# Kernel tuning notes

Hardware: AMD Instinct MI355X
Metric: run time of the kernel (lower is better)

The kernel has to match this reference:

```python
import jax, jax.numpy as jnp
import numpy as np

EMB = 512
HEADS = 8


def setup_inputs() -> dict:
    key = jax.random.key(0)
    ks = jax.random.split(key, 9)
    b, t, k, h = 4, 2048, EMB, HEADS
    s = 1.0 / np.sqrt(k)
    x = jax.random.normal(ks[0], (b, t, k), dtype=jnp.float32)
    Wq = jax.random.normal(ks[1], (k, h * k), dtype=jnp.float32) * s
    bq = jnp.zeros((h * k,), dtype=jnp.float32)
    Wk = jax.random.normal(ks[2], (k, h * k), dtype=jnp.float32) * s
    bk = jnp.zeros((h * k,), dtype=jnp.float32)
    Wv = jax.random.normal(ks[3], (k, h * k), dtype=jnp.float32) * s
    bv = jnp.zeros((h * k,), dtype=jnp.float32)
    Wo = jax.random.normal(ks[4], (h * k, k), dtype=jnp.float32) * (1.0 / np.sqrt(h * k))
    bo = jnp.zeros((k,), dtype=jnp.float32)
    return {"x": x, "Wq": Wq, "bq": bq, "Wk": Wk, "bk": bk,
            "Wv": Wv, "bv": bv, "Wo": Wo, "bo": bo}


def reference(x, Wq, bq, Wk, bk, Wv, bv, Wo, bo):
    b, t, k = x.shape
    h = Wq.shape[1] // k
    scale = k ** (-0.25)  # applied to both q and k, matching /= k**(1/4)
    # projections: [b,t,k] -> [b,t,h,k] -> [b,h,t,k]
    q = (x @ Wq + bq).reshape(b, t, h, k).transpose(0, 2, 1, 3) * scale
    kk = (x @ Wk + bk).reshape(b, t, h, k).transpose(0, 2, 1, 3) * scale
    v = (x @ Wv + bv).reshape(b, t, h, k).transpose(0, 2, 1, 3)
    # attention scores [b,h,t,t]
    scores = jnp.einsum('bhqk,bhsk->bhqs', q, kk)
    w = jax.nn.softmax(scores, axis=-1)
    out = jnp.einsum('bhqs,bhsk->bhqk', w, v)  # [b,h,t,k]
    out = out.transpose(0, 2, 1, 3).reshape(b, t, h * k)
    return out @ Wo + bo
```

## Files before the change

### kernel.cpp

```cpp
#include <hip/hip_runtime.h>
#include <hip/hip_bf16.h>
#include <stdint.h>

typedef __hip_bfloat16 bf16;
typedef __bf16 bf16x8 __attribute__((ext_vector_type(8)));
typedef float floatx4 __attribute__((ext_vector_type(4)));

#define AS_LDS __attribute__((address_space(3)))
#define AS_GLB __attribute__((address_space(1)))

__device__ __forceinline__ void gload_lds16(const bf16* g, bf16* l) {
    __builtin_amdgcn_global_load_lds((const AS_GLB void*)g, (AS_LDS void*)l, 16, 0, 0);
}

__global__ void probe_dtype(const float* __restrict__ x, int* __restrict__ flag) {
    __shared__ int cnt;
    if (threadIdx.x == 0) cnt = 0;
    __syncthreads();
    int ok = 0;
    for (int i = threadIdx.x; i < 4096; i += 256) {
        float v = x[i];
        if (v == v && fabsf(v) < 1.0e3f) ok++;
    }
    atomicAdd(&cnt, ok);
    __syncthreads();
    if (threadIdx.x == 0) *flag = (cnt > 2048) ? 1 : 0;
}

__global__ __launch_bounds__(256) void zero_f32(float* __restrict__ p, int n) {
    int i = blockIdx.x * 256 + threadIdx.x;
    if (i < n) p[i] = 0.f;
}

__global__ __launch_bounds__(256) void convert_to_bf16(
    const void* __restrict__ in, bf16* __restrict__ out, long n,
    const int* __restrict__ flag)
{
    long i = ((long)blockIdx.x * 256 + threadIdx.x) * 8;
    if (i >= n) return;
    bf16 o[8];
    if (*flag) {
        const float* p = (const float*)in + i;
        float4 a = *(const float4*)p;
        float4 b = *(const float4*)(p + 4);
        o[0] = __float2bfloat16(a.x); o[1] = __float2bfloat16(a.y);
        o[2] = __float2bfloat16(a.z); o[3] = __float2bfloat16(a.w);
        o[4] = __float2bfloat16(b.x); o[5] = __float2bfloat16(b.y);
        o[6] = __float2bfloat16(b.z); o[7] = __float2bfloat16(b.w);
    } else {
        *(float4*)o = *(const float4*)((const bf16*)in + i);
    }
    *(float4*)&out[i] = *(float4*)o;
}

__global__ __launch_bounds__(256) void emit_out(
    const bf16* __restrict__ in, void* __restrict__ out, long n,
    const int* __restrict__ flag)
{
    long i = ((long)blockIdx.x * 256 + threadIdx.x) * 8;
    if (i >= n) return;
    bf16 v[8];
    *(float4*)v = *(const float4*)&in[i];
    if (*flag) {
        float* o = (float*)out + i;
        float4 a, b;
        a.x = __bfloat162float(v[0]); a.y = __bfloat162float(v[1]);
        a.z = __bfloat162float(v[2]); a.w = __bfloat162float(v[3]);
        b.x = __bfloat162float(v[4]); b.y = __bfloat162float(v[5]);
        b.z = __bfloat162float(v[6]); b.w = __bfloat162float(v[7]);
        *(float4*)o = a;
        *(float4*)(o + 4) = b;
    } else {
        *(float4*)((bf16*)out + i) = *(float4*)v;
    }
}

__global__ __launch_bounds__(256) void transpose_any(
    const void* __restrict__ inv, bf16* __restrict__ out,
    int ldin, int ldout, const int* __restrict__ flag)
{
    __shared__ bf16 tile[64][80];
    const int fp32 = *flag;
    const int c0 = blockIdx.x * 64;
    const int r0 = blockIdx.y * 64;
    const int tid = threadIdx.x;
#pragma unroll
    for (int it = 0; it < 2; ++it) {
        int ch = tid + it * 256;
        int r = ch >> 3, c = (ch & 7) * 8;
        long eidx = (long)(r0 + r) * ldin + (c0 + c);
        if (fp32) {
            const float* p = (const float*)inv + eidx;
            float4 a = *(const float4*)p;
            float4 b = *(const float4*)(p + 4);
            bf16 o[8];
            o[0] = __float2bfloat16(a.x); o[1] = __float2bfloat16(a.y);
            o[2] = __float2bfloat16(a.z); o[3] = __float2bfloat16(a.w);
            o[4] = __float2bfloat16(b.x); o[5] = __float2bfloat16(b.y);
            o[6] = __float2bfloat16(b.z); o[7] = __float2bfloat16(b.w);
            *(float4*)&tile[r][c] = *(float4*)o;
        } else {
            *(float4*)&tile[r][c] = *(const float4*)((const bf16*)inv + eidx);
        }
    }
    __syncthreads();
#pragma unroll
    for (int it = 0; it < 2; ++it) {
        int ch = tid + it * 256;
        int oc = ch >> 3, rb = (ch & 7) * 8;
        bf16 tmp[8];
#pragma unroll
        for (int i = 0; i < 8; ++i) tmp[i] = tile[rb + i][oc];
        *(float4*)&out[(long)(c0 + oc) * ldout + r0 + rb] = *(float4*)tmp;
    }
}

__global__ __launch_bounds__(256) void transpose_bf16(
    const bf16* __restrict__ in, bf16* __restrict__ out,
    int ldin, int ldout,
    int nz1, long in_z1, long out_z1, long in_z2, long out_z2)
{
    __shared__ bf16 tile[64][80];
    const int z = blockIdx.z;
    const int z1 = z % nz1, z2 = z / nz1;
    in  += (long)z1 * in_z1 + (long)z2 * in_z2;
    out += (long)z1 * out_z1 + (long)z2 * out_z2;
    const int c0 = blockIdx.x * 64;
    const int r0 = blockIdx.y * 64;
    const int tid = threadIdx.x;
#pragma unroll
    for (int it = 0; it < 2; ++it) {
        int ch = tid + it * 256;
        int r = ch >> 3, c = (ch & 7) * 8;
        *(float4*)&tile[r][c] = *(const float4*)&in[(long)(r0 + r) * ldin + c0 + c];
    }
    __syncthreads();
#pragma unroll
    for (int it = 0; it < 2; ++it) {
        int ch = tid + it * 256;
        int oc = ch >> 3, rb = (ch & 7) * 8;
        bf16 tmp[8];
#pragma unroll
        for (int i = 0; i < 8; ++i) tmp[i] = tile[rb + i][oc];
        *(float4*)&out[(long)(c0 + oc) * ldout + r0 + rb] = *(float4*)tmp;
    }
}

template <int MODE, int SWZ>
__global__ __launch_bounds__(512, 2) void gemm256(
    const bf16* __restrict__ A, const bf16* __restrict__ Bt,
    bf16* __restrict__ C, const bf16* __restrict__ bias,
    int lda, int ldb, int ldc,
    long az, long bz, long cz, int K, float scale, int qcols,
    bf16* __restrict__ Vt, int vcol0, float* __restrict__ Lsum)
{
    __shared__ bf16 AsL[2][2][256 * 32];
    __shared__ bf16 BsL[2][2][256 * 32];

    const int tid  = threadIdx.x;
    const int lane = tid & 63;
    const int wave = tid >> 6;
    const int wr = wave >> 2;
    const int wc = wave & 3;
    const int lm = lane & 15;
    const int cl = lane >> 4;

    int bxx = blockIdx.x, byy = blockIdx.y, bzz = blockIdx.z;
    if constexpr (SWZ == 1) {
        int flat = bxx + (byy << 3) + (bzz << 6);
        int xcd = flat & 7, idx = flat >> 3;
        bzz = xcd; bxx = idx & 7; byy = idx >> 3;
    } else if constexpr (SWZ == 2) {
        int flat = bxx + byy * 48;
        int xcd = flat & 7, idx = flat >> 3;
        bxx = xcd * 6 + idx % 6; byy = idx / 6; bzz = 0;
    }
    const long zz = bzz;
    A  += zz * az;
    Bt += zz * bz;
    C  += zz * cz;
    float* Lz = (MODE == 1) ? (Lsum + zz * 2048) : nullptr;
    const int m0 = byy * 256;
    const int n0 = bxx * 256;

    int offA[8], offB[4];
#pragma unroll
    for (int i = 0; i < 8; ++i) {
        int row = wr * 128 + i * 16 + lm;
        offA[i] = row * 32 + ((cl ^ ((row >> 1) & 3)) << 3);
    }
#pragma unroll
    for (int j = 0; j < 4; ++j) {
        int row = wc * 64 + j * 16 + lm;
        offB[j] = row * 32 + ((cl ^ ((row >> 1) & 3)) << 3);
    }

    const int sr = lane >> 2;
    const int sc = lane & 3;
    const int NT = K >> 6;

    floatx4 acc[8][4];
#pragma unroll
    for (int i = 0; i < 8; ++i)
#pragma unroll
        for (int j = 0; j < 4; ++j)
            acc[i][j] = (floatx4){0.f, 0.f, 0.f, 0.f};

    auto stageU = [&](int which, int t, int kh) {
        if (t >= NT) return;
        const bf16* G = which ? Bt : A;
        const int ldg  = which ? ldb : lda;
        const int g0   = which ? n0 : m0;
        bf16* lb = which ? &BsL[t & 1][kh][0] : &AsL[t & 1][kh][0];
        const int kcol = t * 64 + kh * 32;
#pragma unroll
        for (int ii = 0; ii < 2; ++ii) {
            int row = ii * 128 + wave * 16 + sr;
            int cg  = sc ^ ((row >> 1) & 3);
            gload_lds16(G + (long)(g0 + row) * ldg + kcol + cg * 8,
                        lb + row * 32 + sc * 8);
        }
    };

    bf16x8 af[8], bfv[2];
    auto dsA = [&](int b, int kh) {
        const bf16* p = &AsL[b][kh][0];
#pragma unroll
        for (int i = 0; i < 8; ++i) af[i] = *(const bf16x8*)(p + offA[i]);
    };
    auto dsB = [&](int b, int kh, int nh) {
        const bf16* p = &BsL[b][kh][0];
        bfv[0] = *(const bf16x8*)(p + offB[nh * 2]);
        bfv[1] = *(const bf16x8*)(p + offB[nh * 2 + 1]);
    };
    auto mfmaQ = [&](int nh) {
        __builtin_amdgcn_s_setprio(1);
#pragma unroll
        for (int i = 0; i < 8; ++i) {
            acc[i][nh * 2] = __builtin_amdgcn_mfma_f32_16x16x32_bf16(
                af[i], bfv[0], acc[i][nh * 2], 0, 0, 0);
            acc[i][nh * 2 + 1] = __builtin_amdgcn_mfma_f32_16x16x32_bf16(
                af[i], bfv[1], acc[i][nh * 2 + 1], 0, 0, 0);
        }
        __builtin_amdgcn_s_setprio(0);
    };

#define BAR    __builtin_amdgcn_s_barrier()
#define SBZ    __builtin_amdgcn_sched_barrier(0)
#define LGKM0  do { asm volatile("s_waitcnt lgkmcnt(0)" ::: "memory"); SBZ; } while (0)
#define VM(n)  do { asm volatile("s_waitcnt vmcnt(" #n ")" ::: "memory"); SBZ; } while (0)

    stageU(0, 0, 0); stageU(1, 0, 0); stageU(0, 0, 1); stageU(1, 0, 1);
    stageU(0, 1, 0); stageU(1, 1, 0);
    VM(4);
    BAR;

    for (int t0 = 0; t0 < NT; t0 += 2) {
        const bool last = (t0 + 2 >= NT);
        dsA(0, 0); dsB(0, 0, 0); stageU(0, t0 + 1, 1);
        BAR; LGKM0; mfmaQ(0); BAR;
        dsB(0, 0, 1); stageU(1, t0 + 1, 1);
        BAR; LGKM0; mfmaQ(1); BAR;
        dsA(0, 1); dsB(0, 1, 0); stageU(0, t0 + 2, 0);
        BAR; LGKM0; mfmaQ(0); BAR;
        dsB(0, 1, 1); stageU(1, t0 + 2, 0);
        BAR; LGKM0; mfmaQ(1);
        if (last) { VM(0); } else { VM(4); }
        BAR;
        dsA(1, 0); dsB(1, 0, 0); stageU(0, t0 + 2, 1);
        BAR; LGKM0; mfmaQ(0); BAR;
        dsB(1, 0, 1); stageU(1, t0 + 2, 1);
        BAR; LGKM0; mfmaQ(1); BAR;
        dsA(1, 1); dsB(1, 1, 0); stageU(0, t0 + 3, 0);
        BAR; LGKM0; mfmaQ(0); BAR;
        dsB(1, 1, 1); stageU(1, t0 + 3, 0);
        BAR; LGKM0; mfmaQ(1);
        if (!last) { VM(4); }
        BAR;
    }
#undef BAR
#undef SBZ
#undef LGKM0
#undef VM

    const int cr = (lane >> 4) * 4;
    if constexpr (MODE == 1) {
#pragma unroll
        for (int j = 0; j < 4; ++j) {
            long q = n0 + wc * 64 + j * 16 + lm;
            bf16* Cr = C + q * ldc + m0 + wr * 128;
            float rs = 0.f;
#pragma unroll
            for (int i = 0; i < 8; ++i) {
                bf16 pk[4];
#pragma unroll
                for (int r = 0; r < 4; ++r) {
                    float e = __expf(acc[i][j][r]);
                    rs += e;
                    pk[r] = __float2bfloat16(e);
                }
                *(uint64_t*)&Cr[i * 16 + cr] = *(const uint64_t*)pk;
            }
            rs += __shfl_xor(rs, 16);
            rs += __shfl_xor(rs, 32);
            if (cl == 0) atomicAdd(&Lz[q], rs);
        }
    } else {
        if (n0 >= vcol0) {
#pragma unroll
            for (int j = 0; j < 4; ++j) {
                int col = n0 + wc * 64 + j * 16 + lm;
                float bv = __bfloat162float(bias[col]);
                int eg = col - vcol0;
                bf16* vt = Vt + ((long)(eg >> 9) * 512 + (eg & 511)) * 2048;
#pragma unroll
                for (int i = 0; i < 8; ++i) {
                    int t0v = m0 + wr * 128 + i * 16 + cr;
                    bf16 pk[4];
#pragma unroll
                    for (int r = 0; r < 4; ++r)
                        pk[r] = __float2bfloat16(acc[i][j][r] + bv);
                    *(uint64_t*)&vt[t0v] = *(const uint64_t*)pk;
                }
            }
        } else {
            const int l4 = lane & 3;
            float bvj[4], scj[4];
#pragma unroll
            for (int j = 0; j < 4; ++j) {
                int col = n0 + wc * 64 + j * 16 + lm;
                bvj[j] = __bfloat162float(bias[col]);
                scj[j] = (col < qcols) ? scale : 1.0f;
            }
#pragma unroll
            for (int i = 0; i < 8; ++i) {
                int row = m0 + wr * 128 + i * 16 + cr + l4;
                bf16* Cr = C + (long)row * ldc + n0 + wc * 64 + (lm & ~3);
#pragma unroll
                for (int j = 0; j < 4; ++j) {
                    float x0 = (acc[i][j][0] + bvj[j]) * scj[j];
                    float x1 = (acc[i][j][1] + bvj[j]) * scj[j];
                    float x2 = (acc[i][j][2] + bvj[j]) * scj[j];
                    float x3 = (acc[i][j][3] + bvj[j]) * scj[j];
                    float u = __shfl_xor((l4 & 1) ? x0 : x1, 1);
                    float v = __shfl_xor((l4 & 1) ? x2 : x3, 1);
                    if (l4 & 1) { x0 = u; x2 = v; } else { x1 = u; x3 = v; }
                    u = __shfl_xor((l4 & 2) ? x0 : x2, 2);
                    v = __shfl_xor((l4 & 2) ? x1 : x3, 2);
                    if (l4 & 2) { x0 = u; x1 = v; } else { x2 = u; x3 = v; }
                    bf16 pk[4];
                    pk[0] = __float2bfloat16(x0); pk[1] = __float2bfloat16(x1);
                    pk[2] = __float2bfloat16(x2); pk[3] = __float2bfloat16(x3);
                    *(uint64_t*)&Cr[j * 16] = *(const uint64_t*)pk;
                }
            }
        }
    }
}

__global__ __launch_bounds__(512, 2) void gemm_pv(
    const bf16* __restrict__ A, const bf16* __restrict__ Bt,
    bf16* __restrict__ C, const float* __restrict__ L,
    int lda, int ldb, int ldc, long az, long bz, long cz, int K)
{
    __shared__ bf16 AsL[2][2][512 * 32];
    __shared__ bf16 BsL[2][64 * 64];

    const int tid  = threadIdx.x;
    const int lane = tid & 63;
    const int wave = tid >> 6;
    const int wm = wave >> 1;
    const int wn = wave & 1;
    const int lm = lane & 15;
    const int cl = lane >> 4;

    int flat = blockIdx.x + (blockIdx.z << 5);
    const long zz = flat & 7;
    const int qt = flat >> 3;
    A  += zz * az;
    Bt += zz * bz;
    C  += zz * cz;
    const float* Lz = L + zz * 2048;
    const int n0 = qt * 64;

    int offA[8];
#pragma unroll
    for (int i = 0; i < 8; ++i) {
        int row = wm * 128 + i * 16 + lm;
        offA[i] = row * 32 + ((cl ^ ((row >> 1) & 3)) << 3);
    }
    int rB[2], gB0[2];
#pragma unroll
    for (int j = 0; j < 2; ++j) {
        rB[j] = wn * 32 + j * 16 + lm;
        gB0[j] = rB[j] & 7;
    }

    const int sr = lane >> 2;
    const int sc = lane & 3;
    const int NT = K >> 6;

    floatx4 acc[8][2];
#pragma unroll
    for (int i = 0; i < 8; ++i)
#pragma unroll
        for (int j = 0; j < 2; ++j)
            acc[i][j] = (floatx4){0.f, 0.f, 0.f, 0.f};

    auto stageA = [&](int t, int kh) {
        if (t >= NT) return;
        bf16* lb = &AsL[t & 1][kh][0];
        const int kcol = t * 64 + kh * 32;
#pragma unroll
        for (int seg = 0; seg < 4; ++seg) {
            int row = seg * 128 + wave * 16 + sr;
            int cg  = sc ^ ((row >> 1) & 3);
            gload_lds16(A + (long)row * lda + kcol + cg * 8,
                        lb + row * 32 + sc * 8);
        }
    };
    auto stageB = [&](int t) {
        if (t >= NT) return;
        bf16* lb = &BsL[t & 1][0];
        const int kcol = t * 64;
        int row = wave * 8 + (lane >> 3);
        int cg  = (lane & 7) ^ (row & 7);
        gload_lds16(Bt + (long)(n0 + row) * ldb + kcol + cg * 8,
                    lb + row * 64 + (lane & 7) * 8);
    };

    bf16x8 af[8], bfv[2];
    auto dsA = [&](int b, int kh) {
        const bf16* p = &AsL[b][kh][0];
#pragma unroll
        for (int i = 0; i < 8; ++i) af[i] = *(const bf16x8*)(p + offA[i]);
    };
    auto dsB = [&](int b, int kh) {
        const bf16* p = &BsL[b][0];
#pragma unroll
        for (int j = 0; j < 2; ++j) {
            int g = (kh * 4 + cl) ^ gB0[j];
            bfv[j] = *(const bf16x8*)(p + rB[j] * 64 + g * 8);
        }
    };
    auto mfmaQ = [&]() {
        __builtin_amdgcn_s_setprio(1);
#pragma unroll
        for (int i = 0; i < 8; ++i) {
            acc[i][0] = __builtin_amdgcn_mfma_f32_16x16x32_bf16(
                af[i], bfv[0], acc[i][0], 0, 0, 0);
            acc[i][1] = __builtin_amdgcn_mfma_f32_16x16x32_bf16(
                af[i], bfv[1], acc[i][1], 0, 0, 0);
        }
        __builtin_amdgcn_s_setprio(0);
    };

#define BAR    __builtin_amdgcn_s_barrier()
#define SBZ    __builtin_amdgcn_sched_barrier(0)
#define LGKM0  do { asm volatile("s_waitcnt lgkmcnt(0)" ::: "memory"); SBZ; } while (0)
#define VM(n)  do { asm volatile("s_waitcnt vmcnt(" #n ")" ::: "memory"); SBZ; } while (0)

    stageA(0, 0); stageB(0); stageA(0, 1); stageA(1, 0);
    VM(4);
    BAR;

    for (int t0 = 0; t0 < NT; t0 += 2) {
        const bool last = (t0 + 2 >= NT);
        dsA(0, 0); dsB(0, 0); stageA(t0 + 1, 1); stageB(t0 + 1);
        BAR; LGKM0; mfmaQ(); BAR;
        dsA(0, 1); dsB(0, 1); stageA(t0 + 2, 0);
        BAR; LGKM0; mfmaQ();
        if (last) { VM(0); } else { VM(4); }
        BAR;
        dsA(1, 0); dsB(1, 0); stageA(t0 + 2, 1); stageB(t0 + 2);
        BAR; LGKM0; mfmaQ(); BAR;
        dsA(1, 1); dsB(1, 1); stageA(t0 + 3, 0);
        BAR; LGKM0; mfmaQ();
        if (!last) { VM(4); }
        BAR;
    }
#undef BAR
#undef SBZ
#undef LGKM0
#undef VM

#pragma unroll
    for (int j = 0; j < 2; ++j) {
        int col = n0 + wn * 32 + j * 16 + lm;
        float inv = 1.0f / Lz[col];
        bf16* Cr = C + (long)col * ldc + wm * 128;
#pragma unroll
        for (int i = 0; i < 8; ++i) {
            bf16 pk[4];
#pragma unroll
            for (int r = 0; r < 4; ++r)
                pk[r] = __float2bfloat16(acc[i][j][r] * inv);
            *(uint64_t*)&Cr[i * 16 + cl * 4] = *(const uint64_t*)pk;
        }
    }
}

template <int MODE, int SWZ>
__global__ __launch_bounds__(512, 2) void gemm128n(
    const bf16* __restrict__ A, const bf16* __restrict__ Bt,
    bf16* __restrict__ C, const float* __restrict__ L,
    int lda, int ldb, int ldc,
    long az, long bz, long cz, int K, int kper)
{
    __shared__ bf16 AsL[2][2][128 * 32];
    __shared__ bf16 BsL[2][2][256 * 32];

    const int tid  = threadIdx.x;
    const int lane = tid & 63;
    const int wave = tid >> 6;
    const int wr = wave >> 2;
    const int wc = wave & 3;
    const int lm = lane & 15;
    const int cl = lane >> 4;

    int bxx = blockIdx.x, byy = blockIdx.y, bzz = blockIdx.z;
    if constexpr (SWZ == 5) {
        int flat = bxx + (byy << 3) + (bzz << 5);
        int xcd = flat & 7, idx = flat >> 3;
        bzz = xcd; bxx = idx & 7; byy = idx >> 3;
    } else if constexpr (SWZ == 6) {
        int flat = bxx + (byy << 5) + (bzz << 7);
        int nf = (flat & 7) * 32 + (flat >> 3);
        bzz = nf >> 7; int rr = nf & 127; byy = rr >> 5; bxx = rr & 31;
    }
    const long zz = bzz;
    A  += zz * az;
    Bt += zz * bz;
    C  += zz * cz;
    const float* Lz = (MODE == 5) ? (L + zz * 2048) : nullptr;
    const int kbase = (int)(zz * (long)kper);
    const int m0 = byy * 128;
    const int n0 = bxx * 256;

    int offA[4], offB[4];
#pragma unroll
    for (int i = 0; i < 4; ++i) {
        int row = wr * 64 + i * 16 + lm;
        offA[i] = row * 32 + ((cl ^ ((row >> 1) & 3)) << 3);
    }
#pragma unroll
    for (int j = 0; j < 4; ++j) {
        int row = wc * 64 + j * 16 + lm;
        offB[j] = row * 32 + ((cl ^ ((row >> 1) & 3)) << 3);
    }

    const int sr = lane >> 2;
    const int sc = lane & 3;
    const int NT = K >> 6;

    floatx4 acc[4][4];
#pragma unroll
    for (int i = 0; i < 4; ++i)
#pragma unroll
        for (int j = 0; j < 4; ++j)
            acc[i][j] = (floatx4){0.f, 0.f, 0.f, 0.f};

    auto stageA = [&](int t, int kh) {
        if (t >= NT) return;
        bf16* lb = &AsL[t & 1][kh][0];
        const int kcol = kbase + t * 64 + kh * 32;
        int row = wave * 16 + sr;
        int cg  = sc ^ ((row >> 1) & 3);
        gload_lds16(A + (long)(m0 + row) * lda + kcol + cg * 8,
                    lb + row * 32 + sc * 8);
    };
    auto stageB = [&](int t, int kh) {
        if (t >= NT) return;
        bf16* lb = &BsL[t & 1][kh][0];
        const int kcol = kbase + t * 64 + kh * 32;
#pragma unroll
        for (int ii = 0; ii < 2; ++ii) {
            int row = ii * 128 + wave * 16 + sr;
            int cg  = sc ^ ((row >> 1) & 3);
            gload_lds16(Bt + (long)(n0 + row) * ldb + kcol + cg * 8,
                        lb + row * 32 + sc * 8);
        }
    };

    bf16x8 af[4], bfv[2];
    auto dsA = [&](int b, int kh) {
        const bf16* p = &AsL[b][kh][0];
#pragma unroll
        for (int i = 0; i < 4; ++i) af[i] = *(const bf16x8*)(p + offA[i]);
    };
    auto dsB = [&](int b, int kh, int nh) {
        const bf16* p = &BsL[b][kh][0];
        bfv[0] = *(const bf16x8*)(p + offB[nh * 2]);
        bfv[1] = *(const bf16x8*)(p + offB[nh * 2 + 1]);
    };
    auto mfmaQ = [&](int nh) {
        __builtin_amdgcn_s_setprio(1);
#pragma unroll
        for (int i = 0; i < 4; ++i) {
            acc[i][nh * 2] = __builtin_amdgcn_mfma_f32_16x16x32_bf16(
                af[i], bfv[0], acc[i][nh * 2], 0, 0, 0);
            acc[i][nh * 2 + 1] = __builtin_amdgcn_mfma_f32_16x16x32_bf16(
                af[i], bfv[1], acc[i][nh * 2 + 1], 0, 0, 0);
        }
        __builtin_amdgcn_s_setprio(0);
    };

#define BAR    __builtin_amdgcn_s_barrier()
#define SBZ    __builtin_amdgcn_sched_barrier(0)
#define LGKM0  do { asm volatile("s_waitcnt lgkmcnt(0)" ::: "memory"); SBZ; } while (0)
#define VM(n)  do { asm volatile("s_waitcnt vmcnt(" #n ")" ::: "memory"); SBZ; } while (0)

    stageA(0, 0); stageB(0, 0); stageA(0, 1); stageB(0, 1);
    stageA(1, 0); stageB(1, 0);
    VM(3);
    BAR;

    for (int t0 = 0; t0 < NT; t0 += 2) {
        const bool last = (t0 + 2 >= NT);
        dsA(0, 0); dsB(0, 0, 0); stageA(t0 + 1, 1);
        BAR; LGKM0; mfmaQ(0); BAR;
        dsB(0, 0, 1); stageB(t0 + 1, 1);
        BAR; LGKM0; mfmaQ(1); BAR;
        dsA(0, 1); dsB(0, 1, 0); stageA(t0 + 2, 0);
        BAR; LGKM0; mfmaQ(0); BAR;
        dsB(0, 1, 1); stageB(t0 + 2, 0);
        BAR; LGKM0; mfmaQ(1);
        if (last) { VM(0); } else { VM(3); }
        BAR;
        dsA(1, 0); dsB(1, 0, 0); stageA(t0 + 2, 1);
        BAR; LGKM0; mfmaQ(0); BAR;
        dsB(1, 0, 1); stageB(t0 + 2, 1);
        BAR; LGKM0; mfmaQ(1); BAR;
        dsA(1, 1); dsB(1, 1, 0); stageA(t0 + 3, 0);
        BAR; LGKM0; mfmaQ(0); BAR;
        dsB(1, 1, 1); stageB(t0 + 3, 0);
        BAR; LGKM0; mfmaQ(1);
        if (!last) { VM(3); }
        BAR;
    }
#undef BAR
#undef SBZ
#undef LGKM0
#undef VM

    const int cr = cl * 4;
#pragma unroll
    for (int j = 0; j < 4; ++j) {
        int col = n0 + wc * 64 + j * 16 + lm;
        bf16* Cr = C + (long)col * ldc + m0 + wr * 64;
        float inv = 1.0f;
        if constexpr (MODE == 5) inv = 1.0f / Lz[col];
#pragma unroll
        for (int i = 0; i < 4; ++i) {
            bf16 pk[4];
#pragma unroll
            for (int r = 0; r < 4; ++r)
                pk[r] = __float2bfloat16(acc[i][j][r] * inv);
            *(uint64_t*)&Cr[i * 16 + cr] = *(const uint64_t*)pk;
        }
    }
}

template <int MODE, bool SWAP = false, int SWZ = 0>
__global__ __launch_bounds__(256) void gemm_bt(
    const bf16* __restrict__ A, const bf16* __restrict__ Bt,
    bf16* __restrict__ C, const bf16* __restrict__ bias,
    int lda, int ldb, int ldc,
    long az, long bz, long cz, int K, float scale, int qcols,
    bf16* __restrict__ Vt, int vcol0)
{
    __shared__ bf16 As[128 * 64];
    __shared__ bf16 Bs[128 * 64];

    const int tid  = threadIdx.x;
    const int lane = tid & 63;
    const int wave = tid >> 6;
    const int wx = wave & 1;
    const int wy = wave >> 1;

    int bxx = blockIdx.x, byy = blockIdx.y, bzz = blockIdx.z;
    const long zz = bzz;
    A  += zz * az;
    Bt += zz * bz;
    C  += zz * cz;
    const int bm = SWAP ? bxx : byy;
    const int bn = SWAP ? byy : bxx;
    const int m0 = bm * 128;
    const int n0 = bn * 128;

    const int lm = lane & 15;
    const int kq = (lane >> 4) * 8;

    floatx4 acc[4][4];
#pragma unroll
    for (int i = 0; i < 4; ++i)
#pragma unroll
        for (int j = 0; j < 4; ++j)
            acc[i][j] = (floatx4){0.f, 0.f, 0.f, 0.f};

    for (int kt = 0; kt < K; kt += 64) {
        __syncthreads();
#pragma unroll
        for (int it = 0; it < 4; ++it) {
            int ch = tid + it * 256;
            int r = ch >> 3;
            int c = (ch & 7) * 8;
            gload_lds16(A  + (long)(m0 + r) * lda + (kt + c), &As[ch * 8]);
            gload_lds16(Bt + (long)(n0 + r) * ldb + (kt + c), &Bs[ch * 8]);
        }
        __syncthreads();
#pragma unroll
        for (int kk = 0; kk < 64; kk += 32) {
            bf16x8 af[4], bfv[4];
#pragma unroll
            for (int i = 0; i < 4; ++i)
                af[i] = *(const bf16x8*)&As[(wy * 64 + i * 16 + lm) * 64 + kk + kq];
#pragma unroll
            for (int j = 0; j < 4; ++j)
                bfv[j] = *(const bf16x8*)&Bs[(wx * 64 + j * 16 + lm) * 64 + kk + kq];
#pragma unroll
            for (int i = 0; i < 4; ++i)
#pragma unroll
                for (int j = 0; j < 4; ++j)
                    acc[i][j] = __builtin_amdgcn_mfma_f32_16x16x32_bf16(
                        af[i], bfv[j], acc[i][j], 0, 0, 0);
        }
    }

    const int cr = (lane >> 4) * 4;
    if constexpr (MODE == 1) {
#pragma unroll
        for (int j = 0; j < 4; ++j) {
            int col = n0 + wx * 64 + j * 16 + lm;
#pragma unroll
            for (int i = 0; i < 4; ++i)
#pragma unroll
                for (int r = 0; r < 4; ++r) {
                    int row = m0 + wy * 64 + i * 16 + cr + r;
                    C[(long)row * ldc + col] = __float2bfloat16(__expf(acc[i][j][r]));
                }
        }
    } else {
#pragma unroll
        for (int j = 0; j < 4; ++j) {
            int col = n0 + wx * 64 + j * 16 + lm;
            float bv = (MODE == 0 && bias) ? __bfloat162float(bias[col]) : 0.f;
            float sc = (col < qcols) ? scale : 1.0f;
#pragma unroll
            for (int i = 0; i < 4; ++i) {
#pragma unroll
                for (int r = 0; r < 4; ++r) {
                    int row = m0 + wy * 64 + i * 16 + cr + r;
                    long idx = (long)row * ldc + col;
                    float v;
                    if (MODE == 2) v = acc[i][j][r] + __bfloat162float(C[idx]);
                    else           v = (acc[i][j][r] + bv) * sc;
                    C[idx] = __float2bfloat16(v);
                }
            }
        }
    }
}

template <bool SWAP = false>
__global__ __launch_bounds__(256) void gemm_bt_splitk(
    const bf16* __restrict__ A, const bf16* __restrict__ Bt,
    bf16* __restrict__ P, int lda, int ldb, int ldp,
    long az, long bz, long pz, long skStride, int nsk, int Kc)
{
    __shared__ bf16 As[128 * 64];
    __shared__ bf16 Bs[128 * 64];

    const int tid  = threadIdx.x;
    const int lane = tid & 63;
    const int wave = tid >> 6;
    const int wx = wave & 1;
    const int wy = wave >> 1;
    const int zz = blockIdx.z;
    const int ks = zz % nsk;
    const int zh = zz / nsk;
    A  += (long)zh * az;
    Bt += (long)zh * bz;
    bf16* Pz = P + (long)zh * pz + (long)ks * skStride;
    const int bm = SWAP ? blockIdx.x : blockIdx.y;
    const int bn = SWAP ? blockIdx.y : blockIdx.x;
    const int m0 = bm * 128;
    const int n0 = bn * 128;
    const int k0 = ks * Kc;

    const int lm = lane & 15;
    const int kq = (lane >> 4) * 8;

    floatx4 acc[4][4];
#pragma unroll
    for (int i = 0; i < 4; ++i)
#pragma unroll
        for (int j = 0; j < 4; ++j)
            acc[i][j] = (floatx4){0.f, 0.f, 0.f, 0.f};

    for (int kt = k0; kt < k0 + Kc; kt += 64) {
        __syncthreads();
#pragma unroll
        for (int it = 0; it < 4; ++it) {
            int ch = tid + it * 256;
            int r = ch >> 3;
            int c = (ch & 7) * 8;
            gload_lds16(A  + (long)(m0 + r) * lda + (kt + c), &As[ch * 8]);
            gload_lds16(Bt + (long)(n0 + r) * ldb + (kt + c), &Bs[ch * 8]);
        }
        __syncthreads();
#pragma unroll
        for (int kk = 0; kk < 64; kk += 32) {
            bf16x8 af[4], bfv[4];
#pragma unroll
            for (int i = 0; i < 4; ++i)
                af[i] = *(const bf16x8*)&As[(wy * 64 + i * 16 + lm) * 64 + kk + kq];
#pragma unroll
            for (int j = 0; j < 4; ++j)
                bfv[j] = *(const bf16x8*)&Bs[(wx * 64 + j * 16 + lm) * 64 + kk + kq];
#pragma unroll
            for (int i = 0; i < 4; ++i)
#pragma unroll
                for (int j = 0; j < 4; ++j)
                    acc[i][j] = __builtin_amdgcn_mfma_f32_16x16x32_bf16(
                        af[i], bfv[j], acc[i][j], 0, 0, 0);
        }
    }

    const int cr = (lane >> 4) * 4;
#pragma unroll
    for (int j = 0; j < 4; ++j) {
        int col = n0 + wx * 64 + j * 16 + lm;
#pragma unroll
        for (int i = 0; i < 4; ++i)
#pragma unroll
            for (int r = 0; r < 4; ++r) {
                int row = m0 + wy * 64 + i * 16 + cr + r;
                Pz[(long)row * ldp + col] = __float2bfloat16(acc[i][j][r]);
            }
    }
}

__global__ __launch_bounds__(256) void reduce_emit(
    const bf16* __restrict__ P, const bf16* __restrict__ bias,
    void* __restrict__ out, long MN, int N,
    const int* __restrict__ flag)
{
    long i = ((long)blockIdx.x * 256 + threadIdx.x) * 8;
    if (i >= MN) return;
    bf16 bb[8], a[8], b[8];
    *(float4*)bb = *(const float4*)&bias[i & (N - 1)];
    *(float4*)a  = *(const float4*)&P[i];
    *(float4*)b  = *(const float4*)&P[MN + i];
    float s[8];
#pragma unroll
    for (int k = 0; k < 8; ++k)
        s[k] = __bfloat162float(bb[k]) + __bfloat162float(a[k]) + __bfloat162float(b[k]);
    if (*flag) {
        float* o = (float*)out + i;
        float4 lo = {s[0], s[1], s[2], s[3]};
        float4 hi = {s[4], s[5], s[6], s[7]};
        *(float4*)o = lo;
        *(float4*)(o + 4) = hi;
    } else {
        bf16 o[8];
#pragma unroll
        for (int k = 0; k < 8; ++k) o[k] = __float2bfloat16(s[k]);
        *(float4*)&((bf16*)out)[i] = *(float4*)o;
    }
}

__global__ __launch_bounds__(256) void reduce_splitk(
    const bf16* __restrict__ P, const bf16* __restrict__ bias,
    bf16* __restrict__ Out, long MN, int N, int SK)
{
    long i = ((long)blockIdx.x * 256 + threadIdx.x) * 8;
    if (i >= MN) return;
    float s[8];
    if (bias) {
        bf16 bb[8];
        *(float4*)bb = *(const float4*)&bias[i & (N - 1)];
#pragma unroll
        for (int k = 0; k < 8; ++k) s[k] = __bfloat162float(bb[k]);
    } else {
#pragma unroll
        for (int k = 0; k < 8; ++k) s[k] = 0.f;
    }
    for (int z = 0; z < SK; ++z) {
        bf16 a[8];
        *(float4*)a = *(const float4*)&P[(long)z * MN + i];
#pragma unroll
        for (int k = 0; k < 8; ++k) s[k] += __bfloat162float(a[k]);
    }
    bf16 o[8];
#pragma unroll
    for (int k = 0; k < 8; ++k) o[k] = __float2bfloat16(s[k]);
    *(float4*)&Out[i] = *(float4*)o;
}

__global__ __launch_bounds__(256) void softmax_rows2048(bf16* __restrict__ S)
{
    __shared__ float red[8];
    const long row = blockIdx.x;
    bf16* p = S + row * 2048;
    const int tid = threadIdx.x;
    float4 raw = *(const float4*)&p[tid * 8];
    bf16 vb[8];
    *(float4*)vb = raw;
    float v[8];
#pragma unroll
    for (int i = 0; i < 8; ++i) v[i] = __bfloat162float(vb[i]);
    float m = v[0];
#pragma unroll
    for (int i = 1; i < 8; ++i) m = fmaxf(m, v[i]);
#pragma unroll
    for (int o = 32; o > 0; o >>= 1) m = fmaxf(m, __shfl_xor(m, o));
    if ((tid & 63) == 0) red[tid >> 6] = m;
    __syncthreads();
    m = fmaxf(fmaxf(red[0], red[1]), fmaxf(red[2], red[3]));
    float s = 0.f;
#pragma unroll
    for (int i = 0; i < 8; ++i) { v[i] = __expf(v[i] - m); s += v[i]; }
#pragma unroll
    for (int o = 32; o > 0; o >>= 1) s += __shfl_xor(s, o);
    if ((tid & 63) == 0) red[4 + (tid >> 6)] = s;
    __syncthreads();
    s = (red[4] + red[5]) + (red[6] + red[7]);
    float inv = 1.f / s;
#pragma unroll
    for (int i = 0; i < 8; ++i) vb[i] = __float2bfloat16(v[i] * inv);
    *(float4*)&p[tid * 8] = *(float4*)vb;
}

extern "C" void kernel_launch(void* const* d_in, const int* in_sizes, int n_in,
                              void* d_out, int out_size, void* d_ws, size_t ws_size,
                              hipStream_t stream)
{
    const int Bb = 4, T = 2048, E = 512, H = 8;
    const int HE = H * E;
    const int N3 = 3 * HE;
    const int N2 = 2 * HE;
    const int M  = Bb * T;
    const long NX = (long)M * E;

    const void* xr = nullptr;
    const void* Wr[4] = {nullptr, nullptr, nullptr, nullptr};
    const void* br[3] = {nullptr, nullptr, nullptr};
    const void* bor = nullptr;
    int nw = 0, nb = 0;
    for (int i = 0; i < n_in; ++i) {
        int s = in_sizes[i];
        if      (s == (int)NX)      xr = d_in[i];
        else if (s == E * HE)       { if (nw < 4) Wr[nw++] = d_in[i]; }
        else if (s == HE)           { if (nb < 3) br[nb++] = d_in[i]; }
        else if (s == E)            bor = d_in[i];
    }
    if (!xr || nw < 4 || nb < 3 || !bor) {
        xr = d_in[0]; Wr[0] = d_in[1]; br[0] = d_in[2]; Wr[1] = d_in[3];
        br[1] = d_in[4]; Wr[2] = d_in[5]; br[2] = d_in[6]; Wr[3] = d_in[7];
        bor = d_in[8];
    }

    const float qscale = 0.04419417382415922f;
    const int   QC = 1 << 30;
    dim3 blk(256);

    bf16* pool = (bf16*)d_ws;
    int*  flag = (int*)(void*)pool;
    bf16* xc   = pool + 8;
    bf16* bqc  = xc  + NX;
    bf16* bkc  = bqc + HE;
    bf16* bvc  = bkc + HE;
    bf16* boc  = bvc + HE;
    bf16* WqT  = boc + E;
    const size_t w2m = (size_t)E * HE;
    bf16* WkT  = WqT + w2m;
    bf16* WvT  = WkT + w2m;
    bf16* WoT  = WvT + w2m;
    bf16* Ofin = WoT + w2m;
    bf16* p0   = Ofin + NX;

    const size_t wsE    = ws_size / sizeof(bf16);
    const size_t fixedE = (size_t)(p0 - pool);
    const size_t wQK   = (size_t)T * N2;
    const size_t wQKV  = (size_t)T * N3;
    const size_t wBat  = (size_t)T * HE;
    const size_t wHd   = (size_t)T * E;
    const size_t sAll  = (size_t)H * T * T;
    const size_t sOne  = (size_t)T * T;
    const size_t wBig  = (size_t)M * HE;
    const size_t wL    = 32768;
    const size_t needB2 = fixedE + wQK + wBat + sAll + wBig + wL;
    const size_t needB  = fixedE + wQKV + 2 * wBat + sAll;
    const size_t needC  = fixedE + 5 * wBat + sOne;
    const size_t needD  = fixedE + 5 * wHd  + sOne;
    if (wsE < needD) return;

    probe_dtype<<<dim3(1), blk, 0, stream>>>((const float*)xr, flag);
    convert_to_bf16<<<dim3((unsigned)((NX / 8 + 255) / 256)), blk, 0, stream>>>(
        xr, xc, NX, flag);
    convert_to_bf16<<<dim3(2), blk, 0, stream>>>(br[0], bqc, HE, flag);
    convert_to_bf16<<<dim3(2), blk, 0, stream>>>(br[1], bkc, HE, flag);
    convert_to_bf16<<<dim3(2), blk, 0, stream>>>(br[2], bvc, HE, flag);
    convert_to_bf16<<<dim3(1), blk, 0, stream>>>(bor, boc, E, flag);
    transpose_any<<<dim3(HE / 64, E / 64, 1), blk, 0, stream>>>(Wr[0], WqT, HE, E, flag);
    transpose_any<<<dim3(HE / 64, E / 64, 1), blk, 0, stream>>>(Wr[1], WkT, HE, E, flag);
    transpose_any<<<dim3(HE / 64, E / 64, 1), blk, 0, stream>>>(Wr[2], WvT, HE, E, flag);
    transpose_any<<<dim3(E / 64, HE / 64, 1), blk, 0, stream>>>(Wr[3], WoT, E, HE, flag);

    if (wsE >= needB2) {
        bf16* QKb = p0;
        bf16* Vtb = QKb + wQK;
        bf16* S   = Vtb + wBat;
        bf16* Oatt = S + sAll;
        float* Lbuf = (float*)(Oatt + wBig);

        for (int b = 0; b < Bb; ++b) {
            const bf16* xb = xc + (size_t)b * T * E;
            gemm256<4, 2><<<dim3(N3 / 256, T / 256, 1), dim3(512), 0, stream>>>(
                xb, WqT, QKb, bqc, E, E, N2, 0, 0, 0, E, qscale, HE, Vtb, N2,
                nullptr);
            zero_f32<<<dim3(64), blk, 0, stream>>>(Lbuf, H * T);
            gemm256<1, 1><<<dim3(T / 256, T / 256, H), dim3(512), 0, stream>>>(
                QKb + HE, QKb, S, nullptr, N2, N2, T,
                (long)E, (long)E, (long)T * T, E, 1.f, QC, nullptr, 0, Lbuf);
            gemm_pv<<<dim3(T / 64, 1, H), dim3(512), 0, stream>>>(
                Vtb, S, Oatt + (size_t)b * T * HE, Lbuf, T, T, HE,
                (long)E * T, (long)T * T, (long)E, T);
        }
        gemm128n<6, 6><<<dim3(M / 256, E / 128, 2), dim3(512), 0, stream>>>(
            WoT, Oatt, QKb, nullptr, HE, HE, E,
            0, 0, (long)M * E, HE / 2, HE / 2);
        reduce_emit<<<dim3((unsigned)((NX / 8 + 255) / 256)), blk, 0, stream>>>(
            QKb, boc, d_out, NX, E, flag);
        return;
    }

    if (wsE >= needB) {
        bf16* QKVb = p0;
        bf16* Vtb  = QKVb + wQKV;
        bf16* Oatt = Vtb + wBat;
        bf16* S    = Oatt + wBat;

        for (int b = 0; b < Bb; ++b) {
            const bf16* xb = xc + (size_t)b * T * E;
            gemm_bt<0><<<dim3(N3 / 128, T / 128, 1), blk, 0, stream>>>(
                xb, WqT, QKVb, bqc, E, E, N3, 0, 0, 0, E, qscale, HE, nullptr, 0);
            transpose_bf16<<<dim3(E / 64, T / 64, H), blk, 0, stream>>>(
                QKVb + 2 * HE, Vtb, N3, T, H, (long)E, (long)E * T, 0, 0);
            gemm_bt<0><<<dim3(T / 128, T / 128, H), blk, 0, stream>>>(
                QKVb, QKVb + HE, S, nullptr, N3, N3, T,
                (long)E, (long)E, (long)T * T, E, 1.f, QC, nullptr, 0);
            softmax_rows2048<<<dim3(H * T, 1, 1), blk, 0, stream>>>(S);
            gemm_bt<0><<<dim3(E / 128, T / 128, H), blk, 0, stream>>>(
                S, Vtb, Oatt, nullptr, T, T, HE,
                (long)T * T, (long)E * T, (long)E, T, 1.f, QC, nullptr, 0);
            gemm_bt_splitk<false><<<dim3(E / 128, T / 128, 8), blk, 0, stream>>>(
                Oatt, WoT, (bf16*)S, HE, HE, E, 0, 0, 0, (long)T * E, 8, HE / 8);
            reduce_splitk<<<dim3((unsigned)(((long)T * E / 8 + 255) / 256)), blk, 0, stream>>>(
                (bf16*)S, boc, Ofin + (size_t)b * T * E, (long)T * E, E, 8);
        }
    } else if (wsE >= needC) {
        bf16* Qb  = p0;
        bf16* Kb  = Qb  + wBat;
        bf16* Vb  = Kb  + wBat;
        bf16* Vtb = Vb  + wBat;
        bf16* Ob  = Vtb + wBat;
        bf16* S   = Ob  + wBat;

        for (int b = 0; b < Bb; ++b) {
            const bf16* xb = xc + (size_t)b * T * E;
            gemm_bt<0><<<dim3(HE / 128, T / 128, 1), blk, 0, stream>>>(
                xb, WqT, Qb, bqc, E, E, HE, 0, 0, 0, E, qscale, QC, nullptr, 0);
            gemm_bt<0><<<dim3(HE / 128, T / 128, 1), blk, 0, stream>>>(
                xb, WkT, Kb, bkc, E, E, HE, 0, 0, 0, E, 1.f, QC, nullptr, 0);
            gemm_bt<0><<<dim3(HE / 128, T / 128, 1), blk, 0, stream>>>(
                xb, WvT, Vb, bvc, E, E, HE, 0, 0, 0, E, 1.f, QC, nullptr, 0);
            transpose_bf16<<<dim3(E / 64, T / 64, H), blk, 0, stream>>>(
                Vb, Vtb, HE, T, H, (long)E, (long)E * T, 0, 0);
            for (int h = 0; h < H; ++h) {
                gemm_bt<0><<<dim3(T / 128, T / 128, 1), blk, 0, stream>>>(
                    Qb + (size_t)h * E, Kb + (size_t)h * E, S, nullptr,
                    HE, HE, T, 0, 0, 0, E, 1.f, QC, nullptr, 0);
                softmax_rows2048<<<dim3(T, 1, 1), blk, 0, stream>>>(S);
                gemm_bt<0><<<dim3(E / 128, T / 128, 1), blk, 0, stream>>>(
                    S, Vtb + (size_t)h * E * T, Ob + (size_t)h * E, nullptr,
                    T, T, HE, 0, 0, 0, T, 1.f, QC, nullptr, 0);
            }
            gemm_bt<0><<<dim3(E / 128, T / 128, 1), blk, 0, stream>>>(
                Ob, WoT, Ofin + (size_t)b * T * E, boc,
                HE, HE, E, 0, 0, 0, HE, 1.f, QC, nullptr, 0);
        }
    } else {
        bf16* Qh  = p0;
        bf16* Kh  = Qh  + wHd;
        bf16* Vh  = Kh  + wHd;
        bf16* Vth = Vh  + wHd;
        bf16* Oh  = Vth + wHd;
        bf16* S   = Oh  + wHd;

        for (int b = 0; b < Bb; ++b) {
            const bf16* xb = xc + (size_t)b * T * E;
            bf16* outb = Ofin + (size_t)b * T * E;
            for (int h = 0; h < H; ++h) {
                const size_t hw = (size_t)h * E * E;
                gemm_bt<0><<<dim3(E / 128, T / 128, 1), blk, 0, stream>>>(
                    xb, WqT + hw, Qh, bqc + (size_t)h * E, E, E, E,
                    0, 0, 0, E, qscale, QC, nullptr, 0);
                gemm_bt<0><<<dim3(E / 128, T / 128, 1), blk, 0, stream>>>(
                    xb, WkT + hw, Kh, bkc + (size_t)h * E, E, E, E,
                    0, 0, 0, E, 1.f, QC, nullptr, 0);
                gemm_bt<0><<<dim3(E / 128, T / 128, 1), blk, 0, stream>>>(
                    xb, WvT + hw, Vh, bvc + (size_t)h * E, E, E, E,
                    0, 0, 0, E, 1.f, QC, nullptr, 0);
                transpose_bf16<<<dim3(E / 64, T / 64, 1), blk, 0, stream>>>(
                    Vh, Vth, E, T, 1, 0, 0, 0, 0);
                gemm_bt<0><<<dim3(T / 128, T / 128, 1), blk, 0, stream>>>(
                    Qh, Kh, S, nullptr, E, E, T, 0, 0, 0, E, 1.f, QC, nullptr, 0);
                softmax_rows2048<<<dim3(T, 1, 1), blk, 0, stream>>>(S);
                gemm_bt<0><<<dim3(E / 128, T / 128, 1), blk, 0, stream>>>(
                    S, Vth, Oh, nullptr, T, T, E, 0, 0, 0, T, 1.f, QC, nullptr, 0);
                if (h == 0)
                    gemm_bt<0><<<dim3(E / 128, T / 128, 1), blk, 0, stream>>>(
                        Oh, WoT, outb, boc, E, HE, E, 0, 0, 0, E, 1.f, QC, nullptr, 0);
                else
                    gemm_bt<2><<<dim3(E / 128, T / 128, 1), blk, 0, stream>>>(
                        Oh, WoT + (size_t)h * E, outb, nullptr,
                        E, HE, E, 0, 0, 0, E, 1.f, QC, nullptr, 0);
            }
        }
    }

    emit_out<<<dim3((unsigned)((NX / 8 + 255) / 256)), blk, 0, stream>>>(
        Ofin, d_out, NX, flag);
}
```

Baseline: 981.0 us.

## Retile PV GEMM to 256x256 output blocks with split A/B staging

```diff
diff --git a/kernel.cpp b/kernel.cpp
--- a/kernel.cpp
+++ b/kernel.cpp
@@ -358,75 +358,69 @@
     }
 }
 
-__global__ __launch_bounds__(512, 2) void gemm_pv(
+__global__ __launch_bounds__(512, 2) void gemm_pv3(
     const bf16* __restrict__ A, const bf16* __restrict__ Bt,
     bf16* __restrict__ C, const float* __restrict__ L,
     int lda, int ldb, int ldc, long az, long bz, long cz, int K)
 {
-    __shared__ bf16 AsL[2][2][512 * 32];
-    __shared__ bf16 BsL[2][64 * 64];
+    __shared__ bf16 AsL[2][2][256 * 32];
+    __shared__ bf16 BsL[2][2][256 * 32];
 
     const int tid  = threadIdx.x;
     const int lane = tid & 63;
     const int wave = tid >> 6;
-    const int wm = wave >> 1;
-    const int wn = wave & 1;
+    const int wr = wave >> 2;
+    const int wc = wave & 3;
     const int lm = lane & 15;
     const int cl = lane >> 4;
 
-    int flat = blockIdx.x + (blockIdx.z << 5);
-    const long zz = flat & 7;
-    const int qt = flat >> 3;
+    const int bxx = blockIdx.x;
+    const int byy = blockIdx.y;
+    const long zz = blockIdx.z;
     A  += zz * az;
     Bt += zz * bz;
     C  += zz * cz;
     const float* Lz = L + zz * 2048;
-    const int n0 = qt * 64;
-
-    int offA[8];
+    const int m0 = byy * 256;
+    const int n0 = bxx * 256;
+
+    int offA[8], offB[4];
 #pragma unroll
     for (int i = 0; i < 8; ++i) {
-        int row = wm * 128 + i * 16 + lm;
+        int row = wr * 128 + i * 16 + lm;
         offA[i] = row * 32 + ((cl ^ ((row >> 1) & 3)) << 3);
     }
-    int rB[2], gB0[2];
-#pragma unroll
-    for (int j = 0; j < 2; ++j) {
-        rB[j] = wn * 32 + j * 16 + lm;
-        gB0[j] = rB[j] & 7;
+#pragma unroll
+    for (int j = 0; j < 4; ++j) {
+        int row = wc * 64 + j * 16 + lm;
+        offB[j] = row * 32 + ((cl ^ ((row >> 1) & 3)) << 3);
     }
 
     const int sr = lane >> 2;
     const int sc = lane & 3;
     const int NT = K >> 6;
 
-    floatx4 acc[8][2];
+    floatx4 acc[8][4];
 #pragma unroll
     for (int i = 0; i < 8; ++i)
 #pragma unroll
-        for (int j = 0; j < 2; ++j)
+        for (int j = 0; j < 4; ++j)
             acc[i][j] = (floatx4){0.f, 0.f, 0.f, 0.f};
 
-    auto stageA = [&](int t, int kh) {
+    auto stageU = [&](int which, int t, int kh) {
         if (t >= NT) return;
-        bf16* lb = &AsL[t & 1][kh][0];
+        const bf16* G = which ? Bt : A;
+        const int ldg  = which ? ldb : lda;
+        const int g0   = which ? n0 : m0;
+        bf16* lb = which ? &BsL[t & 1][kh][0] : &AsL[t & 1][kh][0];
         const int kcol = t * 64 + kh * 32;
 #pragma unroll
-        for (int seg = 0; seg < 4; ++seg) {
-            int row = seg * 128 + wave * 16 + sr;
+        for (int ii = 0; ii < 2; ++ii) {
+            int row = ii * 128 + wave * 16 + sr;
             int cg  = sc ^ ((row >> 1) & 3);
-            gload_lds16(A + (long)row * lda + kcol + cg * 8,
+            gload_lds16(G + (long)(g0 + row) * ldg + kcol + cg * 8,
                         lb + row * 32 + sc * 8);
         }
-    };
-    auto stageB = [&](int t) {
-        if (t >= NT) return;
-        bf16* lb = &BsL[t & 1][0];
-        const int kcol = t * 64;
-        int row = wave * 8 + (lane >> 3);
-        int cg  = (lane & 7) ^ (row & 7);
-        gload_lds16(Bt + (long)(n0 + row) * ldb + kcol + cg * 8,
-                    lb + row * 64 + (lane & 7) * 8);
     };
 
     bf16x8 af[8], bfv[2];
@@ -435,22 +429,19 @@
 #pragma unroll
         for (int i = 0; i < 8; ++i) af[i] = *(const bf16x8*)(p + offA[i]);
     };
-    auto dsB = [&](int b, int kh) {
-        const bf16* p = &BsL[b][0];
-#pragma unroll
-        for (int j = 0; j < 2; ++j) {
-            int g = (kh * 4 + cl) ^ gB0[j];
-            bfv[j] = *(const bf16x8*)(p + rB[j] * 64 + g * 8);
-        }
-    };
-    auto mfmaQ = [&]() {
+    auto dsB = [&](int b, int kh, int nh) {
+        const bf16* p = &BsL[b][kh][0];
+        bfv[0] = *(const bf16x8*)(p + offB[nh * 2]);
+        bfv[1] = *(const bf16x8*)(p + offB[nh * 2 + 1]);
+    };
+    auto mfmaQ = [&](int nh) {
         __builtin_amdgcn_s_setprio(1);
 #pragma unroll
         for (int i = 0; i < 8; ++i) {
-            acc[i][0] = __builtin_amdgcn_mfma_f32_16x16x32_bf16(
-                af[i], bfv[0], acc[i][0], 0, 0, 0);
-            acc[i][1] = __builtin_amdgcn_mfma_f32_16x16x32_bf16(
-                af[i], bfv[1], acc[i][1], 0, 0, 0);
+            acc[i][nh * 2] = __builtin_amdgcn_mfma_f32_16x16x32_bf16(
+                af[i], bfv[0], acc[i][nh * 2], 0, 0, 0);
+            acc[i][nh * 2 + 1] = __builtin_amdgcn_mfma_f32_16x16x32_bf16(
+                af[i], bfv[1], acc[i][nh * 2 + 1], 0, 0, 0);
         }
         __builtin_amdgcn_s_setprio(0);
     };
@@ -460,22 +451,31 @@
 #define LGKM0  do { asm volatile("s_waitcnt lgkmcnt(0)" ::: "memory"); SBZ; } while (0)
 #define VM(n)  do { asm volatile("s_waitcnt vmcnt(" #n ")" ::: "memory"); SBZ; } while (0)
 
-    stageA(0, 0); stageB(0); stageA(0, 1); stageA(1, 0);
+    stageU(0, 0, 0); stageU(1, 0, 0); stageU(0, 0, 1); stageU(1, 0, 1);
+    stageU(0, 1, 0); stageU(1, 1, 0);
     VM(4);
     BAR;
 
     for (int t0 = 0; t0 < NT; t0 += 2) {
         const bool last = (t0 + 2 >= NT);
-        dsA(0, 0); dsB(0, 0); stageA(t0 + 1, 1); stageB(t0 + 1);
-        BAR; LGKM0; mfmaQ(); BAR;
-        dsA(0, 1); dsB(0, 1); stageA(t0 + 2, 0);
-        BAR; LGKM0; mfmaQ();
+        dsA(0, 0); dsB(0, 0, 0); stageU(0, t0 + 1, 1);
+        BAR; LGKM0; mfmaQ(0); BAR;
+        dsB(0, 0, 1); stageU(1, t0 + 1, 1);
+        BAR; LGKM0; mfmaQ(1); BAR;
+        dsA(0, 1); dsB(0, 1, 0); stageU(0, t0 + 2, 0);
+        BAR; LGKM0; mfmaQ(0); BAR;
+        dsB(0, 1, 1); stageU(1, t0 + 2, 0);
+        BAR; LGKM0; mfmaQ(1);
         if (last) { VM(0); } else { VM(4); }
         BAR;
-        dsA(1, 0); dsB(1, 0); stageA(t0 + 2, 1); stageB(t0 + 2);
-        BAR; LGKM0; mfmaQ(); BAR;
-        dsA(1, 1); dsB(1, 1); stageA(t0 + 3, 0);
-        BAR; LGKM0; mfmaQ();
+        dsA(1, 0); dsB(1, 0, 0); stageU(0, t0 + 2, 1);
+        BAR; LGKM0; mfmaQ(0); BAR;
+        dsB(1, 0, 1); stageU(1, t0 + 2, 1);
+        BAR; LGKM0; mfmaQ(1); BAR;
+        dsA(1, 1); dsB(1, 1, 0); stageU(0, t0 + 3, 0);
+        BAR; LGKM0; mfmaQ(0); BAR;
+        dsB(1, 1, 1); stageU(1, t0 + 3, 0);
+        BAR; LGKM0; mfmaQ(1);
         if (!last) { VM(4); }
         BAR;
     }
@@ -484,18 +484,19 @@
 #undef LGKM0
 #undef VM
 
-#pragma unroll
-    for (int j = 0; j < 2; ++j) {
-        int col = n0 + wn * 32 + j * 16 + lm;
-        float inv = 1.0f / Lz[col];
-        bf16* Cr = C + (long)col * ldc + wm * 128;
+    const int cr = (lane >> 4) * 4;
+#pragma unroll
+    for (int j = 0; j < 4; ++j) {
+        long q = n0 + wc * 64 + j * 16 + lm;
+        float inv = 1.0f / Lz[q];
+        bf16* Cr = C + q * ldc + m0 + wr * 128;
 #pragma unroll
         for (int i = 0; i < 8; ++i) {
             bf16 pk[4];
 #pragma unroll
             for (int r = 0; r < 4; ++r)
                 pk[r] = __float2bfloat16(acc[i][j][r] * inv);
-            *(uint64_t*)&Cr[i * 16 + cl * 4] = *(const uint64_t*)pk;
+            *(uint64_t*)&Cr[i * 16 + cr] = *(const uint64_t*)pk;
         }
     }
 }
@@ -1024,7 +1025,7 @@
             gemm256<1, 1><<<dim3(T / 256, T / 256, H), dim3(512), 0, stream>>>(
                 QKb + HE, QKb, S, nullptr, N2, N2, T,
                 (long)E, (long)E, (long)T * T, E, 1.f, QC, nullptr, 0, Lbuf);
-            gemm_pv<<<dim3(T / 64, 1, H), dim3(512), 0, stream>>>(
+            gemm_pv3<<<dim3(T / 256, E / 256, H), dim3(512), 0, stream>>>(
                 Vtb, S, Oatt + (size_t)b * T * HE, Lbuf, T, T, HE,
                 (long)E * T, (long)T * T, (long)E, T);
         }
```

Measured after the change: 964.4 us. No clear change (-1.7%).
